# Performance work log

Measured on AMD Instinct MI355X. Metric: run time of the kernel, lower is better.

## Reference

```python
import jax, jax.numpy as jnp
import numpy as np

N, E, G = 100000, 400000, 4096
D, H, C, L = 128, 8, 16, 4  # hidden, heads, per-head dim, layers
EPS_BN = 1e-5


def _seg_sum(v, idx, n):
    return jax.ops.segment_sum(v, idx, num_segments=n)


def _seg_max(v, idx, n):
    return jax.ops.segment_max(v, idx, num_segments=n)


def setup_inputs() -> dict:
    key = jax.random.key(0)
    ks = jax.random.split(key, 32)
    rn = lambda k, s, sc=0.1: jax.random.normal(k, s, jnp.float32) * sc
    inp = {
        "x": jax.random.normal(ks[0], (N, 9), jnp.float32),
        "edge_attr": jax.random.normal(ks[1], (E, 3), jnp.float32),
        "edge_index": jax.random.randint(ks[2], (2, E), 0, N, jnp.int32),
        "batch": jnp.sort(jax.random.randint(ks[3], (N,), 0, G, jnp.int32)),
        "W_node": rn(ks[4], (9, D)), "b_node": jnp.zeros((D,), jnp.float32),
        "W_edge": rn(ks[5], (3, D)), "b_edge": jnp.zeros((D,), jnp.float32),
        "W_lin": rn(ks[6], (L, D, D)),
        "att_src": rn(ks[7], (L, H, C)), "att_dst": rn(ks[8], (L, H, C)),
        "W_eproj": rn(ks[9], (L, D, D)), "att_edge": rn(ks[10], (L, H, C)),
        "gat_bias": jnp.zeros((L, D), jnp.float32),
        "bn_gamma": jnp.ones((L, D), jnp.float32), "bn_beta": jnp.zeros((L, D), jnp.float32),
        "gate_W1": rn(ks[11], (D, D // 2)), "gate_b1": jnp.zeros((D // 2,), jnp.float32),
        "gate_W2": rn(ks[12], (D // 2, 1)), "gate_b2": jnp.zeros((1,), jnp.float32),
        "mlp_W1": rn(ks[13], (3 * D, 2 * D)), "mlp_b1": jnp.zeros((2 * D,), jnp.float32),
        "mlp_W2": rn(ks[14], (2 * D, D)), "mlp_b2": jnp.zeros((D,), jnp.float32),
    }
    return inp


def _forward(x, edge_attr, edge_index, batch, W_node, b_node, W_edge, b_edge,
             W_lin, att_src, att_dst, W_eproj, att_edge, gat_bias,
             bn_gamma, bn_beta, gate_W1, gate_b1, gate_W2, gate_b2,
             mlp_W1, mlp_b1, mlp_W2, mlp_b2):
    src, dst = edge_index[0], edge_index[1]
    h = x @ W_node + b_node                         # [N, D]
    e = edge_attr @ W_edge + b_edge                 # [E, D]

    # PyG add_self_loops(fill_value='mean'): self-loop edge feature = mean of
    # incoming edge features at each node.
    deg = _seg_sum(jnp.ones((E,), e.dtype), dst, N)           # [N]
    self_e = _seg_sum(e, dst, N) / jnp.clip(deg, 1.0)[:, None]  # [N, D]
    ar = jnp.arange(N, dtype=src.dtype)
    src_f = jnp.concatenate([src, ar])              # [E+N]
    dst_f = jnp.concatenate([dst, ar])
    e_f = jnp.concatenate([e, self_e], axis=0)      # [E+N, D]

    residual = h
    for l in range(L):
        hp = (h @ W_lin[l]).reshape(N, H, C)                     # [N, H, C]
        a_s = jnp.sum(hp * att_src[l], axis=-1)                  # [N, H]
        a_d = jnp.sum(hp * att_dst[l], axis=-1)                  # [N, H]
        ep = (e_f @ W_eproj[l]).reshape(-1, H, C)                # [E+N, H, C]
        a_e = jnp.sum(ep * att_edge[l], axis=-1)                 # [E+N, H]
        alpha = a_s[src_f] + a_d[dst_f] + a_e
        alpha = jax.nn.leaky_relu(alpha, negative_slope=0.2)
        # segment softmax over edges incident to each destination node
        m = _seg_max(alpha, dst_f, N)
        alpha = jnp.exp(alpha - m[dst_f])
        s = _seg_sum(alpha, dst_f, N)
        alpha = alpha / (s[dst_f] + 1e-16)                       # [E+N, H]
        msg = hp[src_f] * alpha[:, :, None]                      # [E+N, H, C]
        out = _seg_sum(msg, dst_f, N).reshape(N, D) + gat_bias[l]
        # BatchNorm1d (batch statistics, training-style) + ReLU
        mu = jnp.mean(out, axis=0)
        var = jnp.mean((out - mu) ** 2, axis=0)
        out = (out - mu) * jax.lax.rsqrt(var + EPS_BN) * bn_gamma[l] + bn_beta[l]
        out = jax.nn.relu(out)
        if l > 0 and l % 2 == 0:
            out = out + residual
            residual = out
        h = out

    # pooling
    cnt = _seg_sum(jnp.ones((N,), h.dtype), batch, G)            # [G]
    x_mean = _seg_sum(h, batch, G) / jnp.clip(cnt, 1.0)[:, None]
    x_max = _seg_max(h, batch, G)
    x_max = jnp.where(cnt[:, None] > 0, x_max, 0.0)
    gate = jax.nn.relu(h @ gate_W1 + gate_b1) @ gate_W2 + gate_b2  # [N, 1]
    gm = _seg_max(gate[:, 0], batch, G)
    gm = jnp.where(cnt > 0, gm, 0.0)
    ge = jnp.exp(gate[:, 0] - gm[batch])
    gs = _seg_sum(ge, batch, G)
    w = ge / (gs[batch] + 1e-16)
    x_att = _seg_sum(h * w[:, None], batch, G)                   # [G, D]

    gr = jnp.concatenate([x_mean, x_max, x_att], axis=1)         # [G, 3D]
    gr = jax.nn.relu(gr @ mlp_W1 + mlp_b1)
    return jax.nn.relu(gr @ mlp_W2 + mlp_b2)                     # [G, D]


def reference(x, edge_attr, edge_index, batch, W_node, b_node, W_edge, b_edge,
              W_lin, att_src, att_dst, W_eproj, att_edge, gat_bias,
              bn_gamma, bn_beta, gate_W1, gate_b1, gate_W2, gate_b2,
              mlp_W1, mlp_b1, mlp_W2, mlp_b2):
    return _forward(x, edge_attr, edge_index, batch, W_node, b_node, W_edge,
                    b_edge, W_lin, att_src, att_dst, W_eproj, att_edge,
                    gat_bias, bn_gamma, bn_beta, gate_W1, gate_b1, gate_W2,
                    gate_b2, mlp_W1, mlp_b1, mlp_W2, mlp_b2)
```

## Files before the change

kernel.cpp:

```cpp
#include <hip/hip_runtime.h>
#include <math.h>

#define N_NODES 100000
#define N_EDGES 400000
#define N_GRAPH 4096
#define DIM 128
#define HEADS 8
#define CHD 16
#define LAYERS 4
#define EPS_BN 1e-5f
#define BN_BLK 256

__global__ void k_prep(const float* __restrict__ W_eproj, const float* __restrict__ att_edge,
                       const float* __restrict__ W_edge, const float* __restrict__ b_edge,
                       float* __restrict__ small3, float* __restrict__ biasE) {
  __shared__ float sw[DIM * 32];
  int t = threadIdx.x;
  for (int e = t; e < DIM * 32; e += 256) {
    int d = e >> 5, lh = e & 31, l = lh >> 3, hh = lh & 7;
    float s = 0.f;
    const float* wp = W_eproj + ((size_t)l * DIM + d) * DIM + hh * CHD;
    const float* ap = att_edge + (l * HEADS + hh) * CHD;
    #pragma unroll
    for (int c = 0; c < CHD; ++c) s += wp[c] * ap[c];
    sw[e] = s;
  }
  __syncthreads();
  if (t < 96) {
    int l = t / 24, r = t % 24, k = r / 8, hh = r % 8;
    float s = 0.f;
    for (int d = 0; d < DIM; ++d) s += W_edge[k * DIM + d] * sw[d * 32 + l * 8 + hh];
    small3[t] = s;
  } else if (t < 128) {
    int t2 = t - 96, l = t2 / 8, hh = t2 % 8;
    float s = 0.f;
    for (int d = 0; d < DIM; ++d) s += b_edge[d] * sw[d * 32 + l * 8 + hh];
    biasE[t2] = s;
  }
}

__global__ void k_encode(const float* __restrict__ x, const float* __restrict__ Wn,
                         const float* __restrict__ bn, float* __restrict__ hEnc) {
  __shared__ float sw[9 * DIM];
  __shared__ float sb[DIM];
  int t = threadIdx.x;
  for (int i = t; i < 9 * DIM; i += 256) sw[i] = Wn[i];
  if (t < DIM) sb[t] = bn[t];
  __syncthreads();
  size_t id = (size_t)blockIdx.x * 256 + t;
  if (id >= (size_t)N_NODES * DIM) return;
  int n = (int)(id >> 7), d = (int)(id & 127);
  float s = sb[d];
  const float* xr = x + (size_t)n * 9;
  #pragma unroll
  for (int k = 0; k < 9; ++k) s += xr[k] * sw[k * DIM + d];
  hEnc[id] = s;
}

__global__ void k_deg(const int* __restrict__ dst, int* __restrict__ deg) {
  int i = blockIdx.x * 256 + threadIdx.x;
  if (i >= N_EDGES) return;
  atomicAdd(&deg[dst[i]], 1);
}

__global__ void k_scan1(const int* __restrict__ deg, int* __restrict__ rp, int* __restrict__ bsum) {
  __shared__ int s[256];
  int t = threadIdx.x, i = blockIdx.x * 256 + t;
  int v = (i < N_NODES) ? deg[i] : 0;
  s[t] = v;
  __syncthreads();
  for (int off = 1; off < 256; off <<= 1) {
    int u = (t >= off) ? s[t - off] : 0;
    __syncthreads();
    s[t] += u;
    __syncthreads();
  }
  if (i < N_NODES) rp[i] = s[t] - v;
  if (t == 255) bsum[blockIdx.x] = s[255];
}

__global__ void k_scan2(int* __restrict__ bsum, int nb) {
  __shared__ int s[512];
  int t = threadIdx.x;
  int v = (t < nb) ? bsum[t] : 0;
  s[t] = v;
  __syncthreads();
  for (int off = 1; off < 512; off <<= 1) {
    int u = (t >= off) ? s[t - off] : 0;
    __syncthreads();
    s[t] += u;
    __syncthreads();
  }
  if (t < nb) bsum[t] = s[t] - v;
}

__global__ void k_scan3(int* __restrict__ rp, const int* __restrict__ bsum) {
  int i = blockIdx.x * 256 + threadIdx.x;
  if (i < N_NODES) rp[i] += bsum[blockIdx.x];
  if (blockIdx.x == 0 && threadIdx.x == 0) rp[N_NODES] = N_EDGES;
}

__global__ void k_scatter(const int* __restrict__ src, const int* __restrict__ dst,
                          const float* __restrict__ ea, const int* __restrict__ rp,
                          int* __restrict__ fill, int2* __restrict__ cpair,
                          float* __restrict__ cea) {
  int i = blockIdx.x * 256 + threadIdx.x;
  if (i >= N_EDGES) return;
  int d = dst[i];
  int p = rp[d] + atomicAdd(&fill[d], 1);
  cpair[p] = make_int2(src[i], d);
  cea[(size_t)p * 3 + 0] = ea[(size_t)i * 3 + 0];
  cea[(size_t)p * 3 + 1] = ea[(size_t)i * 3 + 1];
  cea[(size_t)p * 3 + 2] = ea[(size_t)i * 3 + 2];
}

__global__ void k_easum(const int* __restrict__ rp, const float* __restrict__ cea,
                        float* __restrict__ easum) {
  int n = blockIdx.x * 256 + threadIdx.x;
  if (n >= N_NODES) return;
  int p0 = rp[n], p1 = rp[n + 1];
  float s0 = 0.f, s1 = 0.f, s2 = 0.f;
  for (int p = p0; p < p1; ++p) {
    s0 += cea[(size_t)p * 3 + 0];
    s1 += cea[(size_t)p * 3 + 1];
    s2 += cea[(size_t)p * 3 + 2];
  }
  easum[n * 3 + 0] = s0;
  easum[n * 3 + 1] = s1;
  easum[n * 3 + 2] = s2;
}

__launch_bounds__(256)
__global__ void k_gemm_hp(const float* __restrict__ hsrc, const float* __restrict__ hEnc,
                          const float* __restrict__ ssv, int mode,
                          const float* __restrict__ W,
                          const float* __restrict__ attS, const float* __restrict__ attD,
                          float* __restrict__ hp, float* __restrict__ a_s,
                          float* __restrict__ a_d) {
  __shared__ float sW[32 * DIM];
  __shared__ float sH[64 * 32];
  int t = threadIdx.x;
  int row0 = blockIdx.x * 64;
  int c0 = (t & 31) * 4;
  int r0 = (t >> 5) * 8;
  float acc[8][4] = {};
  for (int kk = 0; kk < DIM; kk += 32) {
    for (int e = t; e < 1024; e += 256) {
      int row = e >> 5, col4 = (e & 31) << 2;
      *reinterpret_cast<float4*>(&sW[row * DIM + col4]) =
          *reinterpret_cast<const float4*>(W + (size_t)(kk + row) * DIM + col4);
    }
    for (int e = t; e < 512; e += 256) {
      int rr = e >> 3, cc = (e & 7) << 2;
      int grr = row0 + rr;
      int col = kk + cc;
      float4 v = make_float4(0.f, 0.f, 0.f, 0.f);
      if (grr < N_NODES) {
        v = *reinterpret_cast<const float4*>(hsrc + (size_t)grr * DIM + col);
        if (mode >= 1) {
          float4 g = *reinterpret_cast<const float4*>(ssv + col);
          float4 b = *reinterpret_cast<const float4*>(ssv + DIM + col);
          v.x = fmaxf(v.x * g.x + b.x, 0.f);
          v.y = fmaxf(v.y * g.y + b.y, 0.f);
          v.z = fmaxf(v.z * g.z + b.z, 0.f);
          v.w = fmaxf(v.w * g.w + b.w, 0.f);
          if (mode == 2) {
            float4 r4 = *reinterpret_cast<const float4*>(hEnc + (size_t)grr * DIM + col);
            v.x += r4.x; v.y += r4.y; v.z += r4.z; v.w += r4.w;
          }
        }
      }
      *reinterpret_cast<float4*>(&sH[rr * 32 + cc]) = v;
    }
    __syncthreads();
    #pragma unroll 2
    for (int k = 0; k < 32; k += 4) {
      float4 w0 = *reinterpret_cast<const float4*>(&sW[(k + 0) * DIM + c0]);
      float4 w1 = *reinterpret_cast<const float4*>(&sW[(k + 1) * DIM + c0]);
      float4 w2 = *reinterpret_cast<const float4*>(&sW[(k + 2) * DIM + c0]);
      float4 w3 = *reinterpret_cast<const float4*>(&sW[(k + 3) * DIM + c0]);
      #pragma unroll
      for (int r = 0; r < 8; ++r) {
        float4 a = *reinterpret_cast<const float4*>(&sH[(r0 + r) * 32 + k]);
        acc[r][0] += a.x * w0.x; acc[r][0] += a.y * w1.x; acc[r][0] += a.z * w2.x; acc[r][0] += a.w * w3.x;
        acc[r][1] += a.x * w0.y; acc[r][1] += a.y * w1.y; acc[r][1] += a.z * w2.y; acc[r][1] += a.w * w3.y;
        acc[r][2] += a.x * w0.z; acc[r][2] += a.y * w1.z; acc[r][2] += a.z * w2.z; acc[r][2] += a.w * w3.z;
        acc[r][3] += a.x * w0.w; acc[r][3] += a.y * w1.w; acc[r][3] += a.z * w2.w; acc[r][3] += a.w * w3.w;
      }
    }
    __syncthreads();
  }
  int head = c0 >> 4;
  int cin = c0 & 15;
  const float* ap = attS + head * CHD + cin;
  const float* dp = attD + head * CHD + cin;
  float asw0 = ap[0], asw1 = ap[1], asw2 = ap[2], asw3 = ap[3];
  float adw0 = dp[0], adw1 = dp[1], adw2 = dp[2], adw3 = dp[3];
  #pragma unroll
  for (int r = 0; r < 8; ++r) {
    float ps = acc[r][0] * asw0 + acc[r][1] * asw1 + acc[r][2] * asw2 + acc[r][3] * asw3;
    float pd = acc[r][0] * adw0 + acc[r][1] * adw1 + acc[r][2] * adw2 + acc[r][3] * adw3;
    ps += __shfl_xor(ps, 1); ps += __shfl_xor(ps, 2);
    pd += __shfl_xor(pd, 1); pd += __shfl_xor(pd, 2);
    int n = row0 + r0 + r;
    if (n < N_NODES) {
      *reinterpret_cast<float4*>(hp + (size_t)n * DIM + c0) =
          make_float4(acc[r][0], acc[r][1], acc[r][2], acc[r][3]);
      if ((t & 3) == 0) {
        a_s[(size_t)n * HEADS + head] = ps;
        a_d[(size_t)n * HEADS + head] = pd;
      }
    }
  }
}

__global__ void k_alpha(const int2* __restrict__ cpair, const float* __restrict__ cea,
                        const float* __restrict__ a_s, const float* __restrict__ a_d,
                        const float* __restrict__ easum, const int* __restrict__ rp,
                        const float* __restrict__ small3, const float* __restrict__ biasE,
                        float* __restrict__ alpha, int l) {
  __shared__ float s3[24];
  __shared__ float sb[8];
  int t = threadIdx.x;
  if (t < 24) s3[t] = small3[l * 24 + t];
  else if (t < 32) sb[t - 24] = biasE[l * 8 + (t - 24)];
  __syncthreads();
  size_t i = (size_t)blockIdx.x * 256 + t;
  if (i >= (size_t)(N_EDGES + N_NODES)) return;
  float4 aslo, ashi, adlo, adhi;
  float ae[8];
  if (i < N_EDGES) {
    int2 pr = cpair[i];
    float e0 = cea[i * 3 + 0], e1 = cea[i * 3 + 1], e2 = cea[i * 3 + 2];
    #pragma unroll
    for (int hh = 0; hh < 8; ++hh)
      ae[hh] = e0 * s3[hh] + e1 * s3[8 + hh] + e2 * s3[16 + hh] + sb[hh];
    aslo = *reinterpret_cast<const float4*>(a_s + (size_t)pr.x * 8);
    ashi = *reinterpret_cast<const float4*>(a_s + (size_t)pr.x * 8 + 4);
    adlo = *reinterpret_cast<const float4*>(a_d + (size_t)pr.y * 8);
    adhi = *reinterpret_cast<const float4*>(a_d + (size_t)pr.y * 8 + 4);
  } else {
    int n = (int)(i - N_EDGES);
    float e0 = easum[n * 3 + 0], e1 = easum[n * 3 + 1], e2 = easum[n * 3 + 2];
    float dg = (float)(rp[n + 1] - rp[n]);
    float invd = 1.f / fmaxf(dg, 1.f);
    #pragma unroll
    for (int hh = 0; hh < 8; ++hh)
      ae[hh] = (e0 * s3[hh] + e1 * s3[8 + hh] + e2 * s3[16 + hh] + dg * sb[hh]) * invd;
    aslo = *reinterpret_cast<const float4*>(a_s + (size_t)n * 8);
    ashi = *reinterpret_cast<const float4*>(a_s + (size_t)n * 8 + 4);
    adlo = *reinterpret_cast<const float4*>(a_d + (size_t)n * 8);
    adhi = *reinterpret_cast<const float4*>(a_d + (size_t)n * 8 + 4);
  }
  float as8[8] = {aslo.x, aslo.y, aslo.z, aslo.w, ashi.x, ashi.y, ashi.z, ashi.w};
  float ad8[8] = {adlo.x, adlo.y, adlo.z, adlo.w, adhi.x, adhi.y, adhi.z, adhi.w};
  float o[8];
  #pragma unroll
  for (int hh = 0; hh < 8; ++hh) {
    float v = as8[hh] + ad8[hh] + ae[hh];
    o[hh] = (v > 0.f) ? v : 0.2f * v;
  }
  *reinterpret_cast<float4*>(alpha + i * 8) = make_float4(o[0], o[1], o[2], o[3]);
  *reinterpret_cast<float4*>(alpha + i * 8 + 4) = make_float4(o[4], o[5], o[6], o[7]);
}

__launch_bounds__(256)
__global__ void k_aggregate(const float* __restrict__ hp, const float* __restrict__ alpha,
                            const int* __restrict__ rp, const int2* __restrict__ cpair,
                            const float* __restrict__ gbias, float* __restrict__ out) {
  int wv = threadIdx.x >> 6, lane = threadIdx.x & 63;
  int n = blockIdx.x * 4 + wv;
  if (n >= N_NODES) return;
  int p0 = rp[n], p1 = rp[n + 1];
  int deg = p1 - p0;
  int hh = lane & 7, sub = lane >> 3;
  const float* aself = alpha + (size_t)(N_EDGES + n) * 8;
  float m = aself[hh];
  for (int idx = sub; idx < deg; idx += 8)
    m = fmaxf(m, alpha[(size_t)(p0 + idx) * 8 + hh]);
  m = fmaxf(m, __shfl_xor(m, 8));
  m = fmaxf(m, __shfl_xor(m, 16));
  m = fmaxf(m, __shfl_xor(m, 32));
  int h0 = lane >> 4, h1 = h0 + 4;
  float m0 = __shfl(m, h0), m1 = __shfl(m, h1);
  float s = (sub == 0) ? expf(aself[hh] - m) : 0.f;
  float acc0 = 0.f, acc1 = 0.f;
  for (int j0 = 0; j0 < deg; j0 += 8) {
    int idx = j0 + sub;
    float e = 0.f;
    int myc = 0;
    if (idx < deg) {
      e = expf(alpha[(size_t)(p0 + idx) * 8 + hh] - m);
      myc = cpair[p0 + idx].x;
    }
    s += e;
    int kmax = min(8, deg - j0);
    for (int k = 0; k < kmax; ++k) {
      int sa = __shfl(myc, k * 8);
      float e0 = __shfl(e, k * 8 + h0);
      float e1 = __shfl(e, k * 8 + h1);
      acc0 += e0 * hp[(size_t)sa * DIM + lane];
      acc1 += e1 * hp[(size_t)sa * DIM + 64 + lane];
    }
  }
  s += __shfl_xor(s, 8); s += __shfl_xor(s, 16); s += __shfl_xor(s, 32);
  float inv = 1.f / (s + 1e-16f);
  float i0 = __shfl(inv, h0), i1 = __shfl(inv, h1);
  acc0 += expf(aself[h0] - m0) * hp[(size_t)n * DIM + lane];
  acc1 += expf(aself[h1] - m1) * hp[(size_t)n * DIM + 64 + lane];
  out[(size_t)n * DIM + lane] = acc0 * i0 + gbias[lane];
  out[(size_t)n * DIM + 64 + lane] = acc1 * i1 + gbias[64 + lane];
}

__launch_bounds__(256)
__global__ void k_bnstat(const float* __restrict__ h, double* __restrict__ partial) {
  int t = threadIdx.x;
  int c = t & 127, half = t >> 7;
  double s = 0.0, q = 0.0;
  for (int n = blockIdx.x * 2 + half; n < N_NODES; n += BN_BLK * 2) {
    float v = h[(size_t)n * DIM + c];
    s += (double)v;
    q += (double)v * (double)v;
  }
  __shared__ double sd[512];
  sd[t] = s; sd[256 + t] = q;
  __syncthreads();
  if (t < 128) {
    s = sd[t] + sd[t + 128];
    q = sd[256 + t] + sd[256 + t + 128];
    partial[(size_t)blockIdx.x * 256 + t] = s;
    partial[(size_t)blockIdx.x * 256 + 128 + t] = q;
  }
}

__global__ void k_bnfin(const double* __restrict__ partial, const float* __restrict__ gamma,
                        const float* __restrict__ beta, float* __restrict__ ss) {
  int c = threadIdx.x;
  double s = 0.0, q = 0.0;
  for (int b = 0; b < BN_BLK; ++b) {
    s += partial[(size_t)b * 256 + c];
    q += partial[(size_t)b * 256 + 128 + c];
  }
  double mu = s / (double)N_NODES;
  double var = q / (double)N_NODES - mu * mu;
  if (var < 0.0) var = 0.0;
  float rs = rsqrtf((float)var + EPS_BN);
  float g = gamma[c] * rs;
  ss[c] = g;
  ss[DIM + c] = beta[c] - (float)mu * g;
}

__global__ void k_bnfinal(const float* __restrict__ hAgg, const float* __restrict__ ss,
                          float* __restrict__ hFin) {
  size_t i = (size_t)blockIdx.x * 256 + threadIdx.x;
  if (i >= (size_t)N_NODES * DIM) return;
  int c = (int)(i & 127);
  hFin[i] = fmaxf(hAgg[i] * ss[c] + ss[DIM + c], 0.f);
}

__launch_bounds__(256, 2)
__global__ void k_gate(const float* __restrict__ h, const float* __restrict__ W1,
                       const float* __restrict__ b1, const float* __restrict__ W2,
                       const float* __restrict__ b2, float* __restrict__ gate) {
  __shared__ float sHT[128][64];
  __shared__ float red[16][64];
  int t = threadIdx.x;
  int row0 = blockIdx.x * 64;
  {
    int node = t & 63, kq = t >> 6;
    int gn = row0 + node;
    const float* hr = h + (size_t)gn * DIM + kq * 32;
    #pragma unroll
    for (int c = 0; c < 8; ++c) {
      float4 v = (gn < N_NODES) ? *reinterpret_cast<const float4*>(hr + c * 4)
                                : make_float4(0.f, 0.f, 0.f, 0.f);
      sHT[kq * 32 + c * 4 + 0][node] = v.x;
      sHT[kq * 32 + c * 4 + 1][node] = v.y;
      sHT[kq * 32 + c * 4 + 2][node] = v.z;
      sHT[kq * 32 + c * 4 + 3][node] = v.w;
    }
  }
  __syncthreads();
  int tx = t & 15, ty = t >> 4;
  float acc[4][4] = {};
  for (int k = 0; k < 128; k += 4) {
    float4 a0 = *reinterpret_cast<const float4*>(&sHT[k + 0][tx * 4]);
    float4 a1 = *reinterpret_cast<const float4*>(&sHT[k + 1][tx * 4]);
    float4 a2 = *reinterpret_cast<const float4*>(&sHT[k + 2][tx * 4]);
    float4 a3 = *reinterpret_cast<const float4*>(&sHT[k + 3][tx * 4]);
    float4 b0 = *reinterpret_cast<const float4*>(W1 + (size_t)(k + 0) * 64 + ty * 4);
    float4 b1v = *reinterpret_cast<const float4*>(W1 + (size_t)(k + 1) * 64 + ty * 4);
    float4 b2v = *reinterpret_cast<const float4*>(W1 + (size_t)(k + 2) * 64 + ty * 4);
    float4 b3v = *reinterpret_cast<const float4*>(W1 + (size_t)(k + 3) * 64 + ty * 4);
    const float ar[4][4] = {{a0.x, a0.y, a0.z, a0.w}, {a1.x, a1.y, a1.z, a1.w},
                            {a2.x, a2.y, a2.z, a2.w}, {a3.x, a3.y, a3.z, a3.w}};
    const float br[4][4] = {{b0.x, b0.y, b0.z, b0.w}, {b1v.x, b1v.y, b1v.z, b1v.w},
                            {b2v.x, b2v.y, b2v.z, b2v.w}, {b3v.x, b3v.y, b3v.z, b3v.w}};
    #pragma unroll
    for (int i = 0; i < 4; ++i)
      #pragma unroll
      for (int r = 0; r < 4; ++r)
        #pragma unroll
        for (int c = 0; c < 4; ++c)
          acc[r][c] += ar[i][r] * br[i][c];
  }
  float4 bb = *reinterpret_cast<const float4*>(b1 + ty * 4);
  float4 ww = *reinterpret_cast<const float4*>(W2 + ty * 4);
  #pragma unroll
  for (int r = 0; r < 4; ++r) {
    float p = fmaxf(acc[r][0] + bb.x, 0.f) * ww.x
            + fmaxf(acc[r][1] + bb.y, 0.f) * ww.y
            + fmaxf(acc[r][2] + bb.z, 0.f) * ww.z
            + fmaxf(acc[r][3] + bb.w, 0.f) * ww.w;
    red[ty][tx * 4 + r] = p;
  }
  __syncthreads();
  if (t < 64) {
    float ssum = b2[0];
    #pragma unroll
    for (int g = 0; g < 16; ++g) ssum += red[g][t];
    int n = row0 + t;
    if (n < N_NODES) gate[n] = ssum;
  }
}

__global__ void k_gptr(const int* __restrict__ batch, int* __restrict__ gptr) {
  int g = blockIdx.x * 256 + threadIdx.x;
  if (g > N_GRAPH) return;
  if (g == N_GRAPH) { gptr[g] = N_NODES; return; }
  int lo = 0, hi = N_NODES;
  while (lo < hi) {
    int mid = (lo + hi) >> 1;
    if (batch[mid] < g) lo = mid + 1; else hi = mid;
  }
  gptr[g] = lo;
}

__launch_bounds__(128)
__global__ void k_pool(const float* __restrict__ h, const float* __restrict__ gate,
                       const int* __restrict__ gptr, float* __restrict__ gr) {
  int g = blockIdx.x;
  int t = threadIdx.x;
  int p0 = gptr[g], p1 = gptr[g + 1], cnt = p1 - p0;
  float* out = gr + (size_t)g * 384;
  if (cnt == 0) { out[t] = 0.f; out[128 + t] = 0.f; out[256 + t] = 0.f; return; }
  __shared__ float red[2];
  __shared__ float wbuf[128];
  __shared__ float sgm, sinv;
  float lm = -1e30f;
  for (int n = p0 + t; n < p1; n += 128) lm = fmaxf(lm, gate[n]);
  for (int off = 1; off < 64; off <<= 1) lm = fmaxf(lm, __shfl_xor(lm, off));
  if ((t & 63) == 0) red[t >> 6] = lm;
  __syncthreads();
  if (t == 0) sgm = fmaxf(red[0], red[1]);
  __syncthreads();
  float gm = sgm;
  float ls = 0.f;
  for (int n = p0 + t; n < p1; n += 128) ls += expf(gate[n] - gm);
  for (int off = 1; off < 64; off <<= 1) ls += __shfl_xor(ls, off);
  if ((t & 63) == 0) red[t >> 6] = ls;
  __syncthreads();
  if (t == 0) sinv = 1.f / ((red[0] + red[1]) + 1e-16f);
  __syncthreads();
  float inv = sinv;
  float sm = 0.f, mx = -1e30f, wa = 0.f;
  for (int c0 = p0; c0 < p1; c0 += 128) {
    int lim = min(128, p1 - c0);
    if (t < lim) wbuf[t] = expf(gate[c0 + t] - gm) * inv;
    __syncthreads();
    for (int j = 0; j < lim; ++j) {
      float v = h[(size_t)(c0 + j) * DIM + t];
      sm += v;
      mx = fmaxf(mx, v);
      wa += v * wbuf[j];
    }
    __syncthreads();
  }
  out[t] = sm / (float)cnt;
  out[128 + t] = mx;
  out[256 + t] = wa;
}

__launch_bounds__(256)
__global__ void k_mlp1(const float* __restrict__ gr, const float* __restrict__ W1,
                       const float* __restrict__ b1, float* __restrict__ hid) {
  int j = threadIdx.x;
  int g0 = blockIdx.x * 8;
  float acc[8];
  float bj = b1[j];
  #pragma unroll
  for (int g = 0; g < 8; ++g) acc[g] = bj;
  for (int k = 0; k < 384; ++k) {
    float w = W1[(size_t)k * 256 + j];
    #pragma unroll
    for (int g = 0; g < 8; ++g) acc[g] += gr[(size_t)(g0 + g) * 384 + k] * w;
  }
  #pragma unroll
  for (int g = 0; g < 8; ++g) hid[(size_t)(g0 + g) * 256 + j] = fmaxf(acc[g], 0.f);
}

__launch_bounds__(128)
__global__ void k_mlp2(const float* __restrict__ hid, const float* __restrict__ W2,
                       const float* __restrict__ b2, float* __restrict__ out) {
  int j = threadIdx.x;
  int g0 = blockIdx.x * 8;
  float acc[8];
  float bj = b2[j];
  #pragma unroll
  for (int g = 0; g < 8; ++g) acc[g] = bj;
  for (int k = 0; k < 256; ++k) {
    float w = W2[(size_t)k * DIM + j];
    #pragma unroll
    for (int g = 0; g < 8; ++g) acc[g] += hid[(size_t)(g0 + g) * 256 + k] * w;
  }
  #pragma unroll
  for (int g = 0; g < 8; ++g) out[(size_t)(g0 + g) * DIM + j] = fmaxf(acc[g], 0.f);
}

extern "C" void kernel_launch(void* const* d_in, const int* in_sizes, int n_in,
                              void* d_out, int out_size, void* d_ws, size_t ws_size,
                              hipStream_t stream) {
  const float* x         = (const float*)d_in[0];
  const float* edge_attr = (const float*)d_in[1];
  const int*   eidx      = (const int*)d_in[2];
  const int*   batch     = (const int*)d_in[3];
  const float* W_node    = (const float*)d_in[4];
  const float* b_node    = (const float*)d_in[5];
  const float* W_edge    = (const float*)d_in[6];
  const float* b_edge    = (const float*)d_in[7];
  const float* W_lin     = (const float*)d_in[8];
  const float* att_src   = (const float*)d_in[9];
  const float* att_dst   = (const float*)d_in[10];
  const float* W_eproj   = (const float*)d_in[11];
  const float* att_edge  = (const float*)d_in[12];
  const float* gat_bias  = (const float*)d_in[13];
  const float* bn_gamma  = (const float*)d_in[14];
  const float* bn_beta   = (const float*)d_in[15];
  const float* gate_W1   = (const float*)d_in[16];
  const float* gate_b1   = (const float*)d_in[17];
  const float* gate_W2   = (const float*)d_in[18];
  const float* gate_b2   = (const float*)d_in[19];
  const float* mlp_W1    = (const float*)d_in[20];
  const float* mlp_b1    = (const float*)d_in[21];
  const float* mlp_W2    = (const float*)d_in[22];
  const float* mlp_b2    = (const float*)d_in[23];
  const int* src = eidx;
  const int* dst = eidx + N_EDGES;

  char* p = (char*)d_ws;
  auto take = [&](size_t bytes) -> char* {
    char* r = p;
    p += (bytes + 255) & ~(size_t)255;
    return r;
  };
  float* hEnc   = (float*)take((size_t)N_NODES * DIM * 4);
  float* hAgg   = (float*)take((size_t)N_NODES * DIM * 4);
  float* hp     = (float*)take((size_t)N_NODES * DIM * 4);
  float* alpha  = (float*)take((size_t)(N_EDGES + N_NODES) * 8 * 4);
  float* a_s    = (float*)take((size_t)N_NODES * 8 * 4);
  float* a_d    = (float*)take((size_t)N_NODES * 8 * 4);
  int2*  cpair  = (int2*)take((size_t)N_EDGES * 8);
  float* cea    = (float*)take((size_t)N_EDGES * 3 * 4);
  float* easum  = (float*)take((size_t)N_NODES * 3 * 4);
  char* zbase = p;
  int*   deg    = (int*)take((size_t)N_NODES * 4);
  int*   fill   = (int*)take((size_t)N_NODES * 4);
  size_t zbytes = (size_t)(p - zbase);
  int*   rp     = (int*)take((size_t)(N_NODES + 1) * 4);
  int*   bsum   = (int*)take(1024 * 4);
  float* small3 = (float*)take(96 * 4);
  float* biasE  = (float*)take(32 * 4);
  double* partial = (double*)take((size_t)BN_BLK * 256 * 8);
  float* ssAll  = (float*)take(4 * 256 * 4);
  float* gate   = (float*)take((size_t)N_NODES * 4);
  int*   gptr   = (int*)take((size_t)(N_GRAPH + 1) * 4);
  float* gr     = (float*)take((size_t)N_GRAPH * 384 * 4);
  float* hid    = (float*)take((size_t)N_GRAPH * 256 * 4);

  hipMemsetAsync(zbase, 0, zbytes, stream);
  k_prep<<<1, 256, 0, stream>>>(W_eproj, att_edge, W_edge, b_edge, small3, biasE);
  k_encode<<<(N_NODES * DIM) / 256, 256, 0, stream>>>(x, W_node, b_node, hEnc);
  k_deg<<<(N_EDGES + 255) / 256, 256, 0, stream>>>(dst, deg);
  int nb = (N_NODES + 255) / 256;
  k_scan1<<<nb, 256, 0, stream>>>(deg, rp, bsum);
  k_scan2<<<1, 512, 0, stream>>>(bsum, nb);
  k_scan3<<<nb, 256, 0, stream>>>(rp, bsum);
  k_scatter<<<(N_EDGES + 255) / 256, 256, 0, stream>>>(src, dst, edge_attr, rp, fill, cpair, cea);
  k_easum<<<nb, 256, 0, stream>>>(rp, cea, easum);

  for (int l = 0; l < LAYERS; ++l) {
    const float* hsrc = (l == 0) ? hEnc : hAgg;
    int mode = (l == 0) ? 0 : ((l == 3) ? 2 : 1);
    k_gemm_hp<<<(N_NODES + 63) / 64, 256, 0, stream>>>(
        hsrc, hEnc, ssAll + (l > 0 ? (l - 1) * 256 : 0), mode,
        W_lin + (size_t)l * DIM * DIM,
        att_src + l * HEADS * CHD, att_dst + l * HEADS * CHD, hp, a_s, a_d);
    k_alpha<<<(N_EDGES + N_NODES + 255) / 256, 256, 0, stream>>>(
        cpair, cea, a_s, a_d, easum, rp, small3, biasE, alpha, l);
    k_aggregate<<<(N_NODES + 3) / 4, 256, 0, stream>>>(
        hp, alpha, rp, cpair, gat_bias + l * DIM, hAgg);
    k_bnstat<<<BN_BLK, 256, 0, stream>>>(hAgg, partial);
    k_bnfin<<<1, 128, 0, stream>>>(partial, bn_gamma + l * DIM, bn_beta + l * DIM,
                                   ssAll + l * 256);
  }

  float* hFin = hp;
  k_bnfinal<<<(N_NODES * DIM) / 256, 256, 0, stream>>>(hAgg, ssAll + 3 * 256, hFin);
  k_gate<<<(N_NODES + 63) / 64, 256, 0, stream>>>(hFin, gate_W1, gate_b1, gate_W2, gate_b2, gate);
  k_gptr<<<(N_GRAPH + 1 + 255) / 256, 256, 0, stream>>>(batch, gptr);
  k_pool<<<N_GRAPH, 128, 0, stream>>>(hFin, gate, gptr, gr);
  k_mlp1<<<N_GRAPH / 8, 256, 0, stream>>>(gr, mlp_W1, mlp_b1, hid);
  k_mlp2<<<N_GRAPH / 8, 128, 0, stream>>>(hid, mlp_W2, mlp_b2, (float*)d_out);
}
```

Baseline: 1.139 ms.

## Fuse attention logits into aggregation, retile node GEMM, fold final BN into pooling

Edge attention logits are now computed inside the aggregation kernel instead of being written to a separate alpha buffer. The max-subtraction pass of the softmax is dropped, so each logit is exponentiated directly. The node projection GEMM uses 128-row tiles with 8x8 per-thread outputs for more register reuse. The final batch-norm+ReLU kernel is removed and applied on the fly in the gate and pool kernels. Skipping the max subtraction risks exp overflow for large logits, and the bigger GEMM tile raises register pressure.

```diff
diff --git a/kernel.cpp b/kernel.cpp
--- a/kernel.cpp
+++ b/kernel.cpp
@@ -138,19 +138,24 @@
                           float* __restrict__ hp, float* __restrict__ a_s,
                           float* __restrict__ a_d) {
   __shared__ float sW[32 * DIM];
-  __shared__ float sH[64 * 32];
-  int t = threadIdx.x;
-  int row0 = blockIdx.x * 64;
-  int c0 = (t & 31) * 4;
-  int r0 = (t >> 5) * 8;
-  float acc[8][4] = {};
+  __shared__ float sH[128 * 32];
+  int t = threadIdx.x;
+  int row0 = blockIdx.x * 128;
+  int tx = t & 15, ty = t >> 4;
+  int c0 = tx * 8;
+  int r0 = ty * 8;
+  float acc[8][8] = {};
   for (int kk = 0; kk < DIM; kk += 32) {
-    for (int e = t; e < 1024; e += 256) {
+    #pragma unroll
+    for (int i = 0; i < 4; ++i) {
+      int e = t + i * 256;
       int row = e >> 5, col4 = (e & 31) << 2;
       *reinterpret_cast<float4*>(&sW[row * DIM + col4]) =
           *reinterpret_cast<const float4*>(W + (size_t)(kk + row) * DIM + col4);
     }
-    for (int e = t; e < 512; e += 256) {
+    #pragma unroll
+    for (int i = 0; i < 4; ++i) {
+      int e = t + i * 256;
       int rr = e >> 3, cc = (e & 7) << 2;
       int grr = row0 + rr;
       int col = kk + cc;
@@ -173,40 +178,52 @@
       *reinterpret_cast<float4*>(&sH[rr * 32 + cc]) = v;
     }
     __syncthreads();
-    #pragma unroll 2
     for (int k = 0; k < 32; k += 4) {
-      float4 w0 = *reinterpret_cast<const float4*>(&sW[(k + 0) * DIM + c0]);
-      float4 w1 = *reinterpret_cast<const float4*>(&sW[(k + 1) * DIM + c0]);
-      float4 w2 = *reinterpret_cast<const float4*>(&sW[(k + 2) * DIM + c0]);
-      float4 w3 = *reinterpret_cast<const float4*>(&sW[(k + 3) * DIM + c0]);
+      float4 a[8];
       #pragma unroll
-      for (int r = 0; r < 8; ++r) {
-        float4 a = *reinterpret_cast<const float4*>(&sH[(r0 + r) * 32 + k]);
-        acc[r][0] += a.x * w0.x; acc[r][0] += a.y * w1.x; acc[r][0] += a.z * w2.x; acc[r][0] += a.w * w3.x;
-        acc[r][1] += a.x * w0.y; acc[r][1] += a.y * w1.y; acc[r][1] += a.z * w2.y; acc[r][1] += a.w * w3.y;
-        acc[r][2] += a.x * w0.z; acc[r][2] += a.y * w1.z; acc[r][2] += a.z * w2.z; acc[r][2] += a.w * w3.z;
-        acc[r][3] += a.x * w0.w; acc[r][3] += a.y * w1.w; acc[r][3] += a.z * w2.w; acc[r][3] += a.w * w3.w;
+      for (int r = 0; r < 8; ++r)
+        a[r] = *reinterpret_cast<const float4*>(&sH[(r0 + r) * 32 + k]);
+      #pragma unroll
+      for (int k2 = 0; k2 < 4; ++k2) {
+        float4 wA = *reinterpret_cast<const float4*>(&sW[(k + k2) * DIM + c0]);
+        float4 wB = *reinterpret_cast<const float4*>(&sW[(k + k2) * DIM + c0 + 4]);
+        #pragma unroll
+        for (int r = 0; r < 8; ++r) {
+          float av = (k2 == 0) ? a[r].x : (k2 == 1) ? a[r].y : (k2 == 2) ? a[r].z : a[r].w;
+          acc[r][0] += av * wA.x; acc[r][1] += av * wA.y;
+          acc[r][2] += av * wA.z; acc[r][3] += av * wA.w;
+          acc[r][4] += av * wB.x; acc[r][5] += av * wB.y;
+          acc[r][6] += av * wB.z; acc[r][7] += av * wB.w;
+        }
       }
     }
     __syncthreads();
   }
-  int head = c0 >> 4;
-  int cin = c0 & 15;
-  const float* ap = attS + head * CHD + cin;
-  const float* dp = attD + head * CHD + cin;
-  float asw0 = ap[0], asw1 = ap[1], asw2 = ap[2], asw3 = ap[3];
-  float adw0 = dp[0], adw1 = dp[1], adw2 = dp[2], adw3 = dp[3];
+  int head = tx >> 1;
+  int cin0 = (tx & 1) * 8;
+  float sweights[8], dweights[8];
+  #pragma unroll
+  for (int j = 0; j < 8; ++j) {
+    sweights[j] = attS[head * CHD + cin0 + j];
+    dweights[j] = attD[head * CHD + cin0 + j];
+  }
   #pragma unroll
   for (int r = 0; r < 8; ++r) {
-    float ps = acc[r][0] * asw0 + acc[r][1] * asw1 + acc[r][2] * asw2 + acc[r][3] * asw3;
-    float pd = acc[r][0] * adw0 + acc[r][1] * adw1 + acc[r][2] * adw2 + acc[r][3] * adw3;
-    ps += __shfl_xor(ps, 1); ps += __shfl_xor(ps, 2);
-    pd += __shfl_xor(pd, 1); pd += __shfl_xor(pd, 2);
     int n = row0 + r0 + r;
+    float ps = 0.f, pd = 0.f;
+    #pragma unroll
+    for (int j = 0; j < 8; ++j) {
+      ps += acc[r][j] * sweights[j];
+      pd += acc[r][j] * dweights[j];
+    }
+    ps += __shfl_xor(ps, 1);
+    pd += __shfl_xor(pd, 1);
     if (n < N_NODES) {
       *reinterpret_cast<float4*>(hp + (size_t)n * DIM + c0) =
           make_float4(acc[r][0], acc[r][1], acc[r][2], acc[r][3]);
-      if ((t & 3) == 0) {
+      *reinterpret_cast<float4*>(hp + (size_t)n * DIM + c0 + 4) =
+          make_float4(acc[r][4], acc[r][5], acc[r][6], acc[r][7]);
+      if ((tx & 1) == 0) {
         a_s[(size_t)n * HEADS + head] = ps;
         a_d[(size_t)n * HEADS + head] = pd;
       }
@@ -214,100 +231,63 @@
   }
 }
 
-__global__ void k_alpha(const int2* __restrict__ cpair, const float* __restrict__ cea,
-                        const float* __restrict__ a_s, const float* __restrict__ a_d,
-                        const float* __restrict__ easum, const int* __restrict__ rp,
-                        const float* __restrict__ small3, const float* __restrict__ biasE,
-                        float* __restrict__ alpha, int l) {
-  __shared__ float s3[24];
-  __shared__ float sb[8];
-  int t = threadIdx.x;
-  if (t < 24) s3[t] = small3[l * 24 + t];
-  else if (t < 32) sb[t - 24] = biasE[l * 8 + (t - 24)];
-  __syncthreads();
-  size_t i = (size_t)blockIdx.x * 256 + t;
-  if (i >= (size_t)(N_EDGES + N_NODES)) return;
-  float4 aslo, ashi, adlo, adhi;
-  float ae[8];
-  if (i < N_EDGES) {
-    int2 pr = cpair[i];
-    float e0 = cea[i * 3 + 0], e1 = cea[i * 3 + 1], e2 = cea[i * 3 + 2];
-    #pragma unroll
-    for (int hh = 0; hh < 8; ++hh)
-      ae[hh] = e0 * s3[hh] + e1 * s3[8 + hh] + e2 * s3[16 + hh] + sb[hh];
-    aslo = *reinterpret_cast<const float4*>(a_s + (size_t)pr.x * 8);
-    ashi = *reinterpret_cast<const float4*>(a_s + (size_t)pr.x * 8 + 4);
-    adlo = *reinterpret_cast<const float4*>(a_d + (size_t)pr.y * 8);
-    adhi = *reinterpret_cast<const float4*>(a_d + (size_t)pr.y * 8 + 4);
-  } else {
-    int n = (int)(i - N_EDGES);
-    float e0 = easum[n * 3 + 0], e1 = easum[n * 3 + 1], e2 = easum[n * 3 + 2];
-    float dg = (float)(rp[n + 1] - rp[n]);
-    float invd = 1.f / fmaxf(dg, 1.f);
-    #pragma unroll
-    for (int hh = 0; hh < 8; ++hh)
-      ae[hh] = (e0 * s3[hh] + e1 * s3[8 + hh] + e2 * s3[16 + hh] + dg * sb[hh]) * invd;
-    aslo = *reinterpret_cast<const float4*>(a_s + (size_t)n * 8);
-    ashi = *reinterpret_cast<const float4*>(a_s + (size_t)n * 8 + 4);
-    adlo = *reinterpret_cast<const float4*>(a_d + (size_t)n * 8);
-    adhi = *reinterpret_cast<const float4*>(a_d + (size_t)n * 8 + 4);
-  }
-  float as8[8] = {aslo.x, aslo.y, aslo.z, aslo.w, ashi.x, ashi.y, ashi.z, ashi.w};
-  float ad8[8] = {adlo.x, adlo.y, adlo.z, adlo.w, adhi.x, adhi.y, adhi.z, adhi.w};
-  float o[8];
-  #pragma unroll
-  for (int hh = 0; hh < 8; ++hh) {
-    float v = as8[hh] + ad8[hh] + ae[hh];
-    o[hh] = (v > 0.f) ? v : 0.2f * v;
-  }
-  *reinterpret_cast<float4*>(alpha + i * 8) = make_float4(o[0], o[1], o[2], o[3]);
-  *reinterpret_cast<float4*>(alpha + i * 8 + 4) = make_float4(o[4], o[5], o[6], o[7]);
-}
-
 __launch_bounds__(256)
-__global__ void k_aggregate(const float* __restrict__ hp, const float* __restrict__ alpha,
-                            const int* __restrict__ rp, const int2* __restrict__ cpair,
-                            const float* __restrict__ gbias, float* __restrict__ out) {
-  int wv = threadIdx.x >> 6, lane = threadIdx.x & 63;
+__global__ void k_attagg(const float* __restrict__ hp, const int* __restrict__ rp,
+                         const int2* __restrict__ cpair, const float* __restrict__ cea,
+                         const float* __restrict__ a_s, const float* __restrict__ a_d,
+                         const float* __restrict__ easum, const float* __restrict__ small3,
+                         const float* __restrict__ biasE, const float* __restrict__ gbias,
+                         float* __restrict__ out, int l) {
+  __shared__ float sc[32];
+  int t = threadIdx.x;
+  if (t < 24) sc[t] = small3[l * 24 + t];
+  else if (t < 32) sc[t] = biasE[l * 8 + (t - 24)];
+  __syncthreads();
+  int wv = t >> 6, lane = t & 63;
   int n = blockIdx.x * 4 + wv;
   if (n >= N_NODES) return;
   int p0 = rp[n], p1 = rp[n + 1];
   int deg = p1 - p0;
   int hh = lane & 7, sub = lane >> 3;
-  const float* aself = alpha + (size_t)(N_EDGES + n) * 8;
-  float m = aself[hh];
-  for (int idx = sub; idx < deg; idx += 8)
-    m = fmaxf(m, alpha[(size_t)(p0 + idx) * 8 + hh]);
-  m = fmaxf(m, __shfl_xor(m, 8));
-  m = fmaxf(m, __shfl_xor(m, 16));
-  m = fmaxf(m, __shfl_xor(m, 32));
   int h0 = lane >> 4, h1 = h0 + 4;
-  float m0 = __shfl(m, h0), m1 = __shfl(m, h1);
-  float s = (sub == 0) ? expf(aself[hh] - m) : 0.f;
+  float adh = a_d[(size_t)n * 8 + hh];
+  float dg = (float)deg, invd = 1.f / fmaxf(dg, 1.f);
+  float se0 = easum[n * 3 + 0], se1 = easum[n * 3 + 1], se2 = easum[n * 3 + 2];
+  float aeS = (se0 * sc[hh] + se1 * sc[8 + hh] + se2 * sc[16 + hh] + dg * sc[24 + hh]) * invd;
+  float lgS = a_s[(size_t)n * 8 + hh] + adh + aeS;
+  lgS = (lgS > 0.f) ? lgS : 0.2f * lgS;
+  float eS = expf(lgS);
+  float s = (sub == 0) ? eS : 0.f;
   float acc0 = 0.f, acc1 = 0.f;
   for (int j0 = 0; j0 < deg; j0 += 8) {
     int idx = j0 + sub;
     float e = 0.f;
     int myc = 0;
     if (idx < deg) {
-      e = expf(alpha[(size_t)(p0 + idx) * 8 + hh] - m);
-      myc = cpair[p0 + idx].x;
+      int p = p0 + idx;
+      myc = cpair[p].x;
+      float c0v = cea[(size_t)p * 3 + 0], c1v = cea[(size_t)p * 3 + 1], c2v = cea[(size_t)p * 3 + 2];
+      float ae = c0v * sc[hh] + c1v * sc[8 + hh] + c2v * sc[16 + hh] + sc[24 + hh];
+      float lg = a_s[(size_t)myc * 8 + hh] + adh + ae;
+      lg = (lg > 0.f) ? lg : 0.2f * lg;
+      e = expf(lg);
     }
     s += e;
     int kmax = min(8, deg - j0);
     for (int k = 0; k < kmax; ++k) {
       int sa = __shfl(myc, k * 8);
-      float e0 = __shfl(e, k * 8 + h0);
-      float e1 = __shfl(e, k * 8 + h1);
-      acc0 += e0 * hp[(size_t)sa * DIM + lane];
-      acc1 += e1 * hp[(size_t)sa * DIM + 64 + lane];
+      float w0 = __shfl(e, k * 8 + h0);
+      float w1 = __shfl(e, k * 8 + h1);
+      acc0 += w0 * hp[(size_t)sa * DIM + lane];
+      acc1 += w1 * hp[(size_t)sa * DIM + 64 + lane];
     }
   }
   s += __shfl_xor(s, 8); s += __shfl_xor(s, 16); s += __shfl_xor(s, 32);
   float inv = 1.f / (s + 1e-16f);
   float i0 = __shfl(inv, h0), i1 = __shfl(inv, h1);
-  acc0 += expf(aself[h0] - m0) * hp[(size_t)n * DIM + lane];
-  acc1 += expf(aself[h1] - m1) * hp[(size_t)n * DIM + 64 + lane];
+  float eS0 = __shfl(eS, h0), eS1 = __shfl(eS, h1);
+  acc0 += eS0 * hp[(size_t)n * DIM + lane];
+  acc1 += eS1 * hp[(size_t)n * DIM + 64 + lane];
   out[(size_t)n * DIM + lane] = acc0 * i0 + gbias[lane];
   out[(size_t)n * DIM + 64 + lane] = acc1 * i1 + gbias[64 + lane];
 }
@@ -350,18 +330,11 @@
   ss[DIM + c] = beta[c] - (float)mu * g;
 }
 
-__global__ void k_bnfinal(const float* __restrict__ hAgg, const float* __restrict__ ss,
-                          float* __restrict__ hFin) {
-  size_t i = (size_t)blockIdx.x * 256 + threadIdx.x;
-  if (i >= (size_t)N_NODES * DIM) return;
-  int c = (int)(i & 127);
-  hFin[i] = fmaxf(hAgg[i] * ss[c] + ss[DIM + c], 0.f);
-}
-
 __launch_bounds__(256, 2)
-__global__ void k_gate(const float* __restrict__ h, const float* __restrict__ W1,
-                       const float* __restrict__ b1, const float* __restrict__ W2,
-                       const float* __restrict__ b2, float* __restrict__ gate) {
+__global__ void k_gate(const float* __restrict__ hAgg, const float* __restrict__ ss,
+                       const float* __restrict__ W1, const float* __restrict__ b1,
+                       const float* __restrict__ W2, const float* __restrict__ b2,
+                       float* __restrict__ gate) {
   __shared__ float sHT[128][64];
   __shared__ float red[16][64];
   int t = threadIdx.x;
@@ -369,15 +342,18 @@
   {
     int node = t & 63, kq = t >> 6;
     int gn = row0 + node;
-    const float* hr = h + (size_t)gn * DIM + kq * 32;
+    const float* hr = hAgg + (size_t)gn * DIM + kq * 32;
     #pragma unroll
     for (int c = 0; c < 8; ++c) {
+      int col = kq * 32 + c * 4;
       float4 v = (gn < N_NODES) ? *reinterpret_cast<const float4*>(hr + c * 4)
                                 : make_float4(0.f, 0.f, 0.f, 0.f);
-      sHT[kq * 32 + c * 4 + 0][node] = v.x;
-      sHT[kq * 32 + c * 4 + 1][node] = v.y;
-      sHT[kq * 32 + c * 4 + 2][node] = v.z;
-      sHT[kq * 32 + c * 4 + 3][node] = v.w;
+      float4 g = *reinterpret_cast<const float4*>(ss + col);
+      float4 b = *reinterpret_cast<const float4*>(ss + DIM + col);
+      sHT[col + 0][node] = fmaxf(v.x * g.x + b.x, 0.f);
+      sHT[col + 1][node] = fmaxf(v.y * g.y + b.y, 0.f);
+      sHT[col + 2][node] = fmaxf(v.z * g.z + b.z, 0.f);
+      sHT[col + 3][node] = fmaxf(v.w * g.w + b.w, 0.f);
     }
   }
   __syncthreads();
@@ -437,13 +413,15 @@
 }
 
 __launch_bounds__(128)
-__global__ void k_pool(const float* __restrict__ h, const float* __restrict__ gate,
-                       const int* __restrict__ gptr, float* __restrict__ gr) {
+__global__ void k_pool(const float* __restrict__ hAgg, const float* __restrict__ ss,
+                       const float* __restrict__ gate, const int* __restrict__ gptr,
+                       float* __restrict__ gr) {
   int g = blockIdx.x;
   int t = threadIdx.x;
   int p0 = gptr[g], p1 = gptr[g + 1], cnt = p1 - p0;
   float* out = gr + (size_t)g * 384;
   if (cnt == 0) { out[t] = 0.f; out[128 + t] = 0.f; out[256 + t] = 0.f; return; }
+  float bg = ss[t], bb = ss[DIM + t];
   __shared__ float red[2];
   __shared__ float wbuf[128];
   __shared__ float sgm, sinv;
@@ -469,7 +447,7 @@
     if (t < lim) wbuf[t] = expf(gate[c0 + t] - gm) * inv;
     __syncthreads();
     for (int j = 0; j < lim; ++j) {
-      float v = h[(size_t)(c0 + j) * DIM + t];
+      float v = fmaxf(hAgg[(size_t)(c0 + j) * DIM + t] * bg + bb, 0.f);
       sm += v;
       mx = fmaxf(mx, v);
       wa += v * wbuf[j];
@@ -556,7 +534,6 @@
   float* hEnc   = (float*)take((size_t)N_NODES * DIM * 4);
   float* hAgg   = (float*)take((size_t)N_NODES * DIM * 4);
   float* hp     = (float*)take((size_t)N_NODES * DIM * 4);
-  float* alpha  = (float*)take((size_t)(N_EDGES + N_NODES) * 8 * 4);
   float* a_s    = (float*)take((size_t)N_NODES * 8 * 4);
   float* a_d    = (float*)take((size_t)N_NODES * 8 * 4);
   int2*  cpair  = (int2*)take((size_t)N_EDGES * 8);
@@ -591,24 +568,22 @@
   for (int l = 0; l < LAYERS; ++l) {
     const float* hsrc = (l == 0) ? hEnc : hAgg;
     int mode = (l == 0) ? 0 : ((l == 3) ? 2 : 1);
-    k_gemm_hp<<<(N_NODES + 63) / 64, 256, 0, stream>>>(
+    k_gemm_hp<<<(N_NODES + 127) / 128, 256, 0, stream>>>(
         hsrc, hEnc, ssAll + (l > 0 ? (l - 1) * 256 : 0), mode,
         W_lin + (size_t)l * DIM * DIM,
         att_src + l * HEADS * CHD, att_dst + l * HEADS * CHD, hp, a_s, a_d);
-    k_alpha<<<(N_EDGES + N_NODES + 255) / 256, 256, 0, stream>>>(
-        cpair, cea, a_s, a_d, easum, rp, small3, biasE, alpha, l);
-    k_aggregate<<<(N_NODES + 3) / 4, 256, 0, stream>>>(
-        hp, alpha, rp, cpair, gat_bias + l * DIM, hAgg);
+    k_attagg<<<(N_NODES + 3) / 4, 256, 0, stream>>>(
+        hp, rp, cpair, cea, a_s, a_d, easum, small3, biasE,
+        gat_bias + l * DIM, hAgg, l);
     k_bnstat<<<BN_BLK, 256, 0, stream>>>(hAgg, partial);
     k_bnfin<<<1, 128, 0, stream>>>(partial, bn_gamma + l * DIM, bn_beta + l * DIM,
                                    ssAll + l * 256);
   }
 
-  float* hFin = hp;
-  k_bnfinal<<<(N_NODES * DIM) / 256, 256, 0, stream>>>(hAgg, ssAll + 3 * 256, hFin);
-  k_gate<<<(N_NODES + 63) / 64, 256, 0, stream>>>(hFin, gate_W1, gate_b1, gate_W2, gate_b2, gate);
+  const float* ss3 = ssAll + 3 * 256;
+  k_gate<<<(N_NODES + 63) / 64, 256, 0, stream>>>(hAgg, ss3, gate_W1, gate_b1, gate_W2, gate_b2, gate);
   k_gptr<<<(N_GRAPH + 1 + 255) / 256, 256, 0, stream>>>(batch, gptr);
-  k_pool<<<N_GRAPH, 128, 0, stream>>>(hFin, gate, gptr, gr);
+  k_pool<<<N_GRAPH, 128, 0, stream>>>(hAgg, ss3, gate, gptr, gr);
   k_mlp1<<<N_GRAPH / 8, 256, 0, stream>>>(gr, mlp_W1, mlp_b1, hid);
   k_mlp2<<<N_GRAPH / 8, 128, 0, stream>>>(hid, mlp_W2, mlp_b2, (float*)d_out);
 }
```

After: 1.139 ms. No clear change (-0.0%).
